# Performance work log

Hardware: AMD Instinct MI355X
Metric: run time of the kernel (lower is better)

Reference implementation:

```python
import jax, jax.numpy as jnp
import numpy as np

BATCH, FEAT = 128, 1024
CLS = 500
HID = 512

def setup_inputs() -> dict:
    key = jax.random.key(0)
    ks = jax.random.split(key, 6)
    return {
        "image_feats": jax.random.normal(ks[0], (BATCH, FEAT), dtype=jnp.float32),
        "attributes": jax.random.normal(ks[1], (CLS, FEAT), dtype=jnp.float32),
        "W1": jax.random.normal(ks[2], (HID, 2 * FEAT), dtype=jnp.float32) * 0.02,
        "b1": jax.random.normal(ks[3], (HID,), dtype=jnp.float32) * 0.02,
        "W2": jax.random.normal(ks[4], (1, HID), dtype=jnp.float32) * 0.02,
        "b2": jax.random.normal(ks[5], (1,), dtype=jnp.float32) * 0.02,
    }

def reference(image_feats, attributes, W1, b1, W2, b2):
    feat_dim = image_feats.shape[1]
    # fc1 on cat([img, attr]) == img @ W1[:, :F].T + attr @ W1[:, F:].T + b1
    # computed via broadcast-add, never materializing the (B, C, 2F) concat.
    img_part = image_feats @ W1[:, :feat_dim].T          # (B, HID)
    attr_part = attributes @ W1[:, feat_dim:].T          # (C, HID)
    h = jax.nn.relu(img_part[:, None, :] + attr_part[None, :, :] + b1)  # (B, C, HID)
    out = jax.nn.sigmoid(jnp.einsum('bch,oh->bco', h, W2) + b2)          # (B, C, 1)
    return out[..., 0]  # (B, C)
```

## Files before the change

### kernel.cpp

```cpp
#include <hip/hip_runtime.h>
#include <math.h>

#define BATCH 128
#define FEAT  1024
#define CLS   500
#define HID   512
#define SPLITS 4

constexpr int BM = 64, BN = 64, BK = 16;

__global__ __launch_bounds__(256) void gemm_bt_splitk(
    const float* __restrict__ img, const float* __restrict__ attr,
    const float* __restrict__ W1,
    float* __restrict__ imgP, float* __restrict__ attrP)
{
    __shared__ float As[BK][BM + 4];
    __shared__ float Bs[BK][BN + 4];

    const int t  = threadIdx.x;
    const int z  = blockIdx.z;
    const int n0 = blockIdx.x * BN;

    const float* A;
    float* P;
    int M, boff, m0;
    if (blockIdx.y < 2) {
        A = img;  P = imgP;  M = BATCH; boff = 0;
        m0 = blockIdx.y * BM;
    } else {
        A = attr; P = attrP; M = CLS;  boff = FEAT;
        m0 = (blockIdx.y - 2) * BM;
    }

    const int K   = FEAT;
    const int ldb = 2 * FEAT;
    const int Ks  = K / SPLITS;
    const int kbase = z * Ks;

    const int lrow = t >> 2;
    const int lk   = (t & 3) * 4;

    const int tn = t & 15;
    const int tm = t >> 4;

    float acc[4][4];
    #pragma unroll
    for (int i = 0; i < 4; ++i)
        #pragma unroll
        for (int j = 0; j < 4; ++j) acc[i][j] = 0.f;

    for (int kt = 0; kt < Ks; kt += BK) {
        {
            const int m = m0 + lrow;
            float4 av = make_float4(0.f, 0.f, 0.f, 0.f);
            if (m < M)
                av = *(const float4*)&A[(size_t)m * K + kbase + kt + lk];
            As[lk + 0][lrow] = av.x;
            As[lk + 1][lrow] = av.y;
            As[lk + 2][lrow] = av.z;
            As[lk + 3][lrow] = av.w;

            const int n = n0 + lrow;
            const float4 bv =
                *(const float4*)&W1[(size_t)n * ldb + boff + kbase + kt + lk];
            Bs[lk + 0][lrow] = bv.x;
            Bs[lk + 1][lrow] = bv.y;
            Bs[lk + 2][lrow] = bv.z;
            Bs[lk + 3][lrow] = bv.w;
        }
        __syncthreads();
        #pragma unroll
        for (int k = 0; k < BK; ++k) {
            const float4 a = *(const float4*)&As[k][tm * 4];
            const float4 b = *(const float4*)&Bs[k][tn * 4];
            acc[0][0] = fmaf(a.x, b.x, acc[0][0]);
            acc[0][1] = fmaf(a.x, b.y, acc[0][1]);
            acc[0][2] = fmaf(a.x, b.z, acc[0][2]);
            acc[0][3] = fmaf(a.x, b.w, acc[0][3]);
            acc[1][0] = fmaf(a.y, b.x, acc[1][0]);
            acc[1][1] = fmaf(a.y, b.y, acc[1][1]);
            acc[1][2] = fmaf(a.y, b.z, acc[1][2]);
            acc[1][3] = fmaf(a.y, b.w, acc[1][3]);
            acc[2][0] = fmaf(a.z, b.x, acc[2][0]);
            acc[2][1] = fmaf(a.z, b.y, acc[2][1]);
            acc[2][2] = fmaf(a.z, b.z, acc[2][2]);
            acc[2][3] = fmaf(a.z, b.w, acc[2][3]);
            acc[3][0] = fmaf(a.w, b.x, acc[3][0]);
            acc[3][1] = fmaf(a.w, b.y, acc[3][1]);
            acc[3][2] = fmaf(a.w, b.z, acc[3][2]);
            acc[3][3] = fmaf(a.w, b.w, acc[3][3]);
        }
        __syncthreads();
    }

    float* Pz = P + (size_t)z * M * HID;
    #pragma unroll
    for (int i = 0; i < 4; ++i) {
        const int m = m0 + tm * 4 + i;
        if (m < M) {
            float4 v = make_float4(acc[i][0], acc[i][1], acc[i][2], acc[i][3]);
            *(float4*)&Pz[(size_t)m * HID + n0 + tn * 4] = v;
        }
    }
}

__global__ __launch_bounds__(256) void merge_kernel(
    const float* __restrict__ imgP, const float* __restrict__ attrP,
    const float* __restrict__ b1,
    float* __restrict__ imgF, float* __restrict__ attrF)
{
    const int NIMG  = BATCH * HID;
    const int NATTR = CLS * HID;
    const int idx = blockIdx.x * 256 + threadIdx.x;
    if (idx < NIMG) {
        float s = 0.f;
        #pragma unroll
        for (int zz = 0; zz < SPLITS; ++zz) s += imgP[zz * NIMG + idx];
        imgF[idx] = s + b1[idx & (HID - 1)];
    } else if (idx < NIMG + NATTR) {
        const int j = idx - NIMG;
        float s = 0.f;
        #pragma unroll
        for (int zz = 0; zz < SPLITS; ++zz) s += attrP[zz * NATTR + j];
        attrF[j] = s;
    }
}

constexpr int TB = 16, TC = 16, HC = 256;

__global__ __launch_bounds__(256) void pair_kernel(
    const float* __restrict__ imgF, const float* __restrict__ attrF,
    const float* __restrict__ W2, const float* __restrict__ b2,
    float* __restrict__ out)
{
    __shared__ float U[TB][HC + 4];
    __shared__ float V[TC][HC + 4];
    __shared__ float w2s[HID];

    const int t  = threadIdx.x;
    const int c0 = blockIdx.x * TC;
    const int b0 = blockIdx.y * TB;

    w2s[t]       = W2[t];
    w2s[t + 256] = W2[t + 256];

    const int ci = t & 15;
    const int bi = t >> 4;

    float acc = 0.f;
    for (int hc = 0; hc < HID; hc += HC) {
        __syncthreads();
        #pragma unroll
        for (int rep = 0; rep < 4; ++rep) {
            const int e   = rep * 256 + t;
            const int row = e >> 6;
            const int c4  = (e & 63) * 4;
            *(float4*)&U[row][c4] =
                *(const float4*)&imgF[(b0 + row) * HID + hc + c4];
            const int c = c0 + row;
            float4 v = make_float4(0.f, 0.f, 0.f, 0.f);
            if (c < CLS)
                v = *(const float4*)&attrF[c * HID + hc + c4];
            *(float4*)&V[row][c4] = v;
        }
        __syncthreads();
        #pragma unroll
        for (int h4 = 0; h4 < HC / 4; ++h4) {
            const float4 u = *(const float4*)&U[bi][h4 * 4];
            const float4 v = *(const float4*)&V[ci][h4 * 4];
            const float4 w = *(const float4*)&w2s[hc + h4 * 4];
            acc = fmaf(fmaxf(u.x + v.x, 0.f), w.x, acc);
            acc = fmaf(fmaxf(u.y + v.y, 0.f), w.y, acc);
            acc = fmaf(fmaxf(u.z + v.z, 0.f), w.z, acc);
            acc = fmaf(fmaxf(u.w + v.w, 0.f), w.w, acc);
        }
    }

    const int b = b0 + bi;
    const int c = c0 + ci;
    if (c < CLS) {
        const float x = acc + b2[0];
        out[b * CLS + c] = 1.f / (1.f + __expf(-x));
    }
}

extern "C" void kernel_launch(void* const* d_in, const int* in_sizes, int n_in,
                              void* d_out, int out_size, void* d_ws, size_t ws_size,
                              hipStream_t stream) {
    const float* img  = (const float*)d_in[0];
    const float* attr = (const float*)d_in[1];
    const float* W1   = (const float*)d_in[2];
    const float* b1   = (const float*)d_in[3];
    const float* W2   = (const float*)d_in[4];
    const float* b2   = (const float*)d_in[5];
    float* out = (float*)d_out;

    float* ws    = (float*)d_ws;
    float* imgP  = ws;
    float* attrP = imgP  + (size_t)SPLITS * BATCH * HID;
    float* imgF  = attrP + (size_t)SPLITS * CLS * HID;
    float* attrF = imgF  + (size_t)BATCH * HID;

    dim3 ggrid(HID / BN, 2 + 8, SPLITS);
    gemm_bt_splitk<<<ggrid, 256, 0, stream>>>(img, attr, W1, imgP, attrP);

    const int ntot = BATCH * HID + CLS * HID;
    merge_kernel<<<(ntot + 255) / 256, 256, 0, stream>>>(imgP, attrP, b1, imgF, attrF);

    dim3 pgrid((CLS + TC - 1) / TC, BATCH / TB);
    pair_kernel<<<pgrid, 256, 0, stream>>>(imgF, attrF, W2, b2, out);
}
```

Before: 99.62 us.

## Raise split-K, prefetch GEMM tiles, restructure pair kernel with wave-uniform batch rows

Measured after the change: 110.2 us. 1.11x slower.

```diff
diff --git a/kernel.cpp b/kernel.cpp
--- a/kernel.cpp
+++ b/kernel.cpp
@@ -5,7 +5,7 @@
 #define FEAT  1024
 #define CLS   500
 #define HID   512
-#define SPLITS 4
+#define SPL   8
 
 constexpr int BM = 64, BN = 64, BK = 16;
 
@@ -32,16 +32,24 @@
         m0 = (blockIdx.y - 2) * BM;
     }
 
-    const int K   = FEAT;
-    const int ldb = 2 * FEAT;
-    const int Ks  = K / SPLITS;
-    const int kbase = z * Ks;
+    const int K    = FEAT;
+    const int ldb  = 2 * FEAT;
+    const int Ks   = K / SPL;
+    const int kb   = z * Ks;
 
     const int lrow = t >> 2;
-    const int lk   = (t & 3) * 4;
+    const int lk4  = (t & 3) * 4;
 
     const int tn = t & 15;
     const int tm = t >> 4;
+
+    const bool aok = (m0 + lrow) < M;
+    const float* Arow = A  + (size_t)(m0 + lrow) * K;
+    const float* Brow = W1 + (size_t)(n0 + lrow) * ldb + boff;
+
+    float4 av = aok ? *(const float4*)&Arow[kb + lk4]
+                    : make_float4(0.f, 0.f, 0.f, 0.f);
+    float4 bv = *(const float4*)&Brow[kb + lk4];
 
     float acc[4][4];
     #pragma unroll
@@ -50,25 +58,22 @@
         for (int j = 0; j < 4; ++j) acc[i][j] = 0.f;
 
     for (int kt = 0; kt < Ks; kt += BK) {
-        {
-            const int m = m0 + lrow;
-            float4 av = make_float4(0.f, 0.f, 0.f, 0.f);
-            if (m < M)
-                av = *(const float4*)&A[(size_t)m * K + kbase + kt + lk];
-            As[lk + 0][lrow] = av.x;
-            As[lk + 1][lrow] = av.y;
-            As[lk + 2][lrow] = av.z;
-            As[lk + 3][lrow] = av.w;
-
-            const int n = n0 + lrow;
-            const float4 bv =
-                *(const float4*)&W1[(size_t)n * ldb + boff + kbase + kt + lk];
-            Bs[lk + 0][lrow] = bv.x;
-            Bs[lk + 1][lrow] = bv.y;
-            Bs[lk + 2][lrow] = bv.z;
-            Bs[lk + 3][lrow] = bv.w;
-        }
-        __syncthreads();
+        As[lk4 + 0][lrow] = av.x;
+        As[lk4 + 1][lrow] = av.y;
+        As[lk4 + 2][lrow] = av.z;
+        As[lk4 + 3][lrow] = av.w;
+        Bs[lk4 + 0][lrow] = bv.x;
+        Bs[lk4 + 1][lrow] = bv.y;
+        Bs[lk4 + 2][lrow] = bv.z;
+        Bs[lk4 + 3][lrow] = bv.w;
+        __syncthreads();
+
+        if (kt + BK < Ks) {
+            av = aok ? *(const float4*)&Arow[kb + kt + BK + lk4]
+                     : make_float4(0.f, 0.f, 0.f, 0.f);
+            bv = *(const float4*)&Brow[kb + kt + BK + lk4];
+        }
+
         #pragma unroll
         for (int k = 0; k < BK; ++k) {
             const float4 a = *(const float4*)&As[k][tm * 4];
@@ -115,72 +120,67 @@
     if (idx < NIMG) {
         float s = 0.f;
         #pragma unroll
-        for (int zz = 0; zz < SPLITS; ++zz) s += imgP[zz * NIMG + idx];
+        for (int zz = 0; zz < SPL; ++zz) s += imgP[zz * NIMG + idx];
         imgF[idx] = s + b1[idx & (HID - 1)];
     } else if (idx < NIMG + NATTR) {
         const int j = idx - NIMG;
         float s = 0.f;
         #pragma unroll
-        for (int zz = 0; zz < SPLITS; ++zz) s += attrP[zz * NATTR + j];
+        for (int zz = 0; zz < SPL; ++zz) s += attrP[zz * NATTR + j];
         attrF[j] = s;
     }
 }
 
-constexpr int TB = 16, TC = 16, HC = 256;
+constexpr int PC = 64;
+constexpr int HC = 128;
 
 __global__ __launch_bounds__(256) void pair_kernel(
     const float* __restrict__ imgF, const float* __restrict__ attrF,
     const float* __restrict__ W2, const float* __restrict__ b2,
     float* __restrict__ out)
 {
-    __shared__ float U[TB][HC + 4];
-    __shared__ float V[TC][HC + 4];
-    __shared__ float w2s[HID];
-
-    const int t  = threadIdx.x;
-    const int c0 = blockIdx.x * TC;
-    const int b0 = blockIdx.y * TB;
-
-    w2s[t]       = W2[t];
-    w2s[t + 256] = W2[t + 256];
-
-    const int ci = t & 15;
-    const int bi = t >> 4;
-
-    float acc = 0.f;
+    __shared__ float4 V[(HC / 4) * PC];
+
+    const int t   = threadIdx.x;
+    const int ci  = t & 63;
+    const int wid = __builtin_amdgcn_readfirstlane(t >> 6);
+    const int b   = blockIdx.y * 4 + wid;
+    const int c0  = blockIdx.x * PC;
+
+    const float* up = imgF + (size_t)b * HID;
+
+    float ax = 0.f, ay = 0.f, az = 0.f, aw = 0.f;
+
     for (int hc = 0; hc < HID; hc += HC) {
         __syncthreads();
         #pragma unroll
-        for (int rep = 0; rep < 4; ++rep) {
-            const int e   = rep * 256 + t;
-            const int row = e >> 6;
-            const int c4  = (e & 63) * 4;
-            *(float4*)&U[row][c4] =
-                *(const float4*)&imgF[(b0 + row) * HID + hc + c4];
-            const int c = c0 + row;
+        for (int rep = 0; rep < 8; ++rep) {
+            const int idx = rep * 256 + t;
+            const int r   = idx >> 5;
+            const int f4  = idx & 31;
             float4 v = make_float4(0.f, 0.f, 0.f, 0.f);
-            if (c < CLS)
-                v = *(const float4*)&attrF[c * HID + hc + c4];
-            *(float4*)&V[row][c4] = v;
-        }
-        __syncthreads();
+            if (c0 + r < CLS)
+                v = *(const float4*)&attrF[(size_t)(c0 + r) * HID + hc + f4 * 4];
+            V[f4 * PC + ((r ^ f4) & 63)] = v;
+        }
+        __syncthreads();
+
         #pragma unroll
         for (int h4 = 0; h4 < HC / 4; ++h4) {
-            const float4 u = *(const float4*)&U[bi][h4 * 4];
-            const float4 v = *(const float4*)&V[ci][h4 * 4];
-            const float4 w = *(const float4*)&w2s[hc + h4 * 4];
-            acc = fmaf(fmaxf(u.x + v.x, 0.f), w.x, acc);
-            acc = fmaf(fmaxf(u.y + v.y, 0.f), w.y, acc);
-            acc = fmaf(fmaxf(u.z + v.z, 0.f), w.z, acc);
-            acc = fmaf(fmaxf(u.w + v.w, 0.f), w.w, acc);
-        }
-    }
-
-    const int b = b0 + bi;
+            const float4 v = V[h4 * PC + ((ci ^ h4) & 63)];
+            const float4 u = *(const float4*)&up[hc + h4 * 4];
+            const float4 w = *(const float4*)&W2[hc + h4 * 4];
+            ax = fmaf(fmaxf(u.x + v.x, 0.f), w.x, ax);
+            ay = fmaf(fmaxf(u.y + v.y, 0.f), w.y, ay);
+            az = fmaf(fmaxf(u.z + v.z, 0.f), w.z, az);
+            aw = fmaf(fmaxf(u.w + v.w, 0.f), w.w, aw);
+        }
+    }
+
     const int c = c0 + ci;
     if (c < CLS) {
-        const float x = acc + b2[0];
-        out[b * CLS + c] = 1.f / (1.f + __expf(-x));
+        const float x = (ax + ay) + (az + aw) + b2[0];
+        out[(size_t)b * CLS + c] = 1.f / (1.f + __expf(-x));
     }
 }
 
@@ -197,16 +197,16 @@
 
     float* ws    = (float*)d_ws;
     float* imgP  = ws;
-    float* attrP = imgP  + (size_t)SPLITS * BATCH * HID;
-    float* imgF  = attrP + (size_t)SPLITS * CLS * HID;
+    float* attrP = imgP  + (size_t)SPL * BATCH * HID;
+    float* imgF  = attrP + (size_t)SPL * CLS * HID;
     float* attrF = imgF  + (size_t)BATCH * HID;
 
-    dim3 ggrid(HID / BN, 2 + 8, SPLITS);
+    dim3 ggrid(HID / BN, 2 + 8, SPL);
     gemm_bt_splitk<<<ggrid, 256, 0, stream>>>(img, attr, W1, imgP, attrP);
 
     const int ntot = BATCH * HID + CLS * HID;
     merge_kernel<<<(ntot + 255) / 256, 256, 0, stream>>>(imgP, attrP, b1, imgF, attrF);
 
-    dim3 pgrid((CLS + TC - 1) / TC, BATCH / TB);
+    dim3 pgrid((CLS + PC - 1) / PC, BATCH / 4);
     pair_kernel<<<pgrid, 256, 0, stream>>>(imgF, attrF, W2, b2, out);
 }
```
